# Performance work log

Hardware: AMD Instinct MI355X
Metric: run time of the kernel (lower is better)

## Reference

```python
import jax, jax.numpy as jnp
import numpy as np

D = 100  # embedding_dim (hard-coded in the original module)


def _prelu(x, a):
    return jnp.where(x >= 0, x, a * x)


def setup_inputs() -> dict:
    key = jax.random.key(0)
    ks = jax.random.split(key, 12)
    B, S, L, R, V = 32, 50, 20, 16, 50000
    T = L * R  # tokens per sentence = len_max_sentence * n_routes
    return {
        "stories": jax.random.randint(ks[0], (B, S, T), 0, V),
        "queries": jax.random.randint(ks[1], (B, L), 0, V),
        "emb": 0.1 * jax.random.normal(ks[2], (V, D), dtype=jnp.float32),
        "in_mult": jnp.ones((T, D), dtype=jnp.float32),
        "q_mult": jnp.ones((L, D), dtype=jnp.float32),
        "keys": 0.1 * jax.random.normal(ks[3], (R, D), dtype=jnp.float32),
        "init_state": 0.1 * jax.random.normal(ks[4], (D,), dtype=jnp.float32),
        "U": 0.1 * jax.random.normal(ks[5], (R * D, D), dtype=jnp.float32),
        "Vw": 0.1 * jax.random.normal(ks[6], (R * D, R * D), dtype=jnp.float32),
        "Ww": 0.1 * jax.random.normal(ks[7], (R * D, R * D), dtype=jnp.float32),
        "Hw": 0.1 * jax.random.normal(ks[8], (D, D), dtype=jnp.float32),
        "Rw": 0.1 * jax.random.normal(ks[9], (V, D), dtype=jnp.float32),
        "alpha_in": jnp.ones((1,), dtype=jnp.float32),  # PReLU(init=1)
        "alpha_q": jnp.ones((1,), dtype=jnp.float32),
    }


def reference(stories, queries, emb, in_mult, q_mult, keys, init_state,
              U, Vw, Ww, Hw, Rw, alpha_in, alpha_q):
    B, S, T = stories.shape
    R = keys.shape[0]
    emb0 = emb.at[0].set(0.0)  # padding_idx=0 row is zero
    # stories -> [B,S,T,D] -> route-sum -> [B,S,R,D]
    x = emb0[stories] * in_mult
    x = x.reshape(B, S, R, T // R, D).sum(axis=3)
    # V(keys.flatten()) is constant across timesteps
    v_keys = (keys.reshape(-1) @ Vw.T).reshape(R, D)
    state0 = jnp.tile(init_state[None, None, :], (B, 1, 1))  # [B,1,D]

    def step(state, sent):  # state [B,1,D], sent [B,R,D]
        gate = jax.nn.sigmoid(sent * state + sent * keys)
        u = (state.reshape(B, D) @ U.T).reshape(B, R, D)
        w = (sent.reshape(B, R * D) @ Ww.T).reshape(B, R, D)
        cand = _prelu(u + v_keys + w, alpha_in)
        # null-sentence mask: zero out positions where gate == sigmoid(0) = 0.5
        mask = jax.lax.stop_gradient(jnp.where(gate == 0.5, 0.0, 1.0))
        state = state + (cand * gate * mask).sum(axis=1, keepdims=True)
        # torch.norm over singleton dim=1 (= elementwise abs), kept faithful
        state = state / jnp.sqrt(jnp.sum(state * state, axis=1, keepdims=True))
        return state, None

    state, _ = jax.lax.scan(step, state0, jnp.swapaxes(x, 0, 1))

    q = (emb0[queries] * q_mult).sum(axis=1, keepdims=True)  # [B,1,D]
    h = _prelu(q + (state.reshape(B, D) @ Hw.T).reshape(B, 1, D), alpha_q)
    return h.reshape(B, D) @ Rw.T  # [B, vocab]
```

## Files before the change

### kernel.cpp

```cpp
#include <hip/hip_runtime.h>
#include <cstddef>
#include <cstdint>

#define B_  32
#define S_  50
#define L_  20
#define R_  16
#define D_  100
#define V_  50000
#define T_  320
#define RD_ 1600
#define BS_ 1600
#define NG_ 25
#define NP_ 16

typedef float v4f __attribute__((ext_vector_type(4)));
typedef unsigned short u16;
#define NTL(p)  __builtin_nontemporal_load((const v4f*)(p))

__device__ __forceinline__ float uf(unsigned u) { return __uint_as_float(u); }

__device__ __forceinline__ void bsplit(float a, unsigned& h, unsigned& l) {
  const unsigned bits = __float_as_uint(a);
  const unsigned hb = bits & 0xffff0000u;
  h = hb >> 16;
  l = __float_as_uint(a - __uint_as_float(hb)) >> 16;
}

__device__ __forceinline__ void bsplit4(float4 a, uint2& h, uint2& l) {
  unsigned h0,h1,h2,h3,l0,l1,l2,l3;
  bsplit(a.x, h0, l0); bsplit(a.y, h1, l1);
  bsplit(a.z, h2, l2); bsplit(a.w, h3, l3);
  h.x = h0 | (h1 << 16); h.y = h2 | (h3 << 16);
  l.x = l0 | (l1 << 16); l.y = l2 | (l3 << 16);
}

__global__ __launch_bounds__(512) void setup_kernel(
    const int* __restrict__ stories, const float* __restrict__ emb,
    const float* __restrict__ in_mult, const float* __restrict__ U,
    const float* __restrict__ Vw, const float* __restrict__ keys,
    const float* __restrict__ init_state, const float* __restrict__ Ww,
    float* __restrict__ x,
    u16* __restrict__ wh, u16* __restrict__ wl,
    float* __restrict__ table, float* __restrict__ vk, float* __restrict__ u0)
{
  const int blk = blockIdx.x, tid = threadIdx.x;
  if (blk < 1600) {
    __shared__ int toks[T_];
    const int* st = stories + (size_t)blk * T_;
    if (tid < T_) toks[tid] = st[tid];
    __syncthreads();
    if (tid < 400) {
      const int j4 = tid * 4;
      const int r  = j4 / D_;
      const int d4 = j4 - r * D_;
      float4 acc = make_float4(0.f, 0.f, 0.f, 0.f);
      #pragma unroll
      for (int l = 0; l < 20; ++l) {
        const int t = r * 20 + l;
        const int tok = toks[t];
        if (tok != 0) {
          float4 e = *(const float4*)&emb[(size_t)tok * D_ + d4];
          float4 m = *(const float4*)&in_mult[(size_t)t * D_ + d4];
          acc.x += e.x * m.x; acc.y += e.y * m.y;
          acc.z += e.z * m.z; acc.w += e.w * m.w;
        }
      }
      *(float4*)&x[(size_t)blk * RD_ + j4] = acc;
    }
  } else if (blk < 2000) {
    const int q = blk - 1600;
    const int g = q >> 4, p = q & 15;
    const float s0 = (p & 1) ? -1.f : 1.f;
    const float s1 = (p & 2) ? -1.f : 1.f;
    const float s2 = (p & 4) ? -1.f : 1.f;
    const float s3 = (p & 8) ? -1.f : 1.f;
    if (tid < 400) {
      const int j4 = tid * 4;
      float t[4];
      #pragma unroll
      for (int jj = 0; jj < 4; ++jj) {
        const float* ur = &U[(size_t)(j4 + jj) * D_ + 4 * g];
        t[jj] = s0*ur[0] + s1*ur[1] + s2*ur[2] + s3*ur[3];
      }
      *(float4*)&table[((size_t)(g * NP_ + p)) * RD_ + j4] =
          make_float4(t[0], t[1], t[2], t[3]);
    }
  } else if (blk < 2200) {
    const int wave = tid >> 6, lane = tid & 63;
    const int j = (blk - 2000) * 8 + wave;
    float acc = 0.f;
    for (int k = lane; k < RD_; k += 64)
      acc += keys[k] * Vw[(size_t)j * RD_ + k];
    #pragma unroll
    for (int off = 32; off > 0; off >>= 1) acc += __shfl_down(acc, off);
    if (lane == 0) vk[j] = acc;
  } else if (blk < 2400) {
    const int wave = tid >> 6, lane = tid & 63;
    const int j = (blk - 2200) * 8 + wave;
    const float* Ur = U + (size_t)j * D_;
    float acc = Ur[lane] * init_state[lane];
    if (lane < 36) acc += Ur[64 + lane] * init_state[64 + lane];
    #pragma unroll
    for (int off = 32; off > 0; off >>= 1) acc += __shfl_down(acc, off);
    if (lane == 0) u0[j] = acc;
  } else {
    const int e = ((blk - 2400) * 512 + tid) * 8;
    float4 a0 = *(const float4*)&Ww[e];
    float4 a1 = *(const float4*)&Ww[e + 4];
    uint2 h0, l0, h1, l1;
    bsplit4(a0, h0, l0);
    bsplit4(a1, h1, l1);
    uint4 hv = make_uint4(h0.x, h0.y, h1.x, h1.y);
    uint4 lv = make_uint4(l0.x, l0.y, l1.x, l1.y);
    *(uint4*)&wh[e] = hv;
    *(uint4*)&wl[e] = lv;
  }
}

typedef const __attribute__((address_space(1))) unsigned GAu;
typedef __attribute__((address_space(3))) unsigned LDSu;
#define GLL(SRC, DST) __builtin_amdgcn_global_load_lds((GAu*)(SRC), (LDSu*)(DST), 16, 0, 0)

__device__ __forceinline__ void mfma16(v4f& d, v4f a, v4f b) {
  asm("v_mfma_f32_16x16x32_bf16 %0, %1, %2, %0" : "+v"(d) : "v"(a), "v"(b));
}

__global__ __launch_bounds__(256) void gemm_mfma_kernel(
    const float* __restrict__ A,
    const u16* __restrict__ wh, const u16* __restrict__ wl,
    float* __restrict__ C)
{
  __shared__ __align__(16) char smem[2][4][8192];
  const int tid = threadIdx.x;
  const int lane = tid & 63, wid = tid >> 6;
  const int bm = blockIdx.y * 128, bn = blockIdx.x * 128;

  int ldsoff[2], srcB[2];
  #pragma unroll
  for (int i = 0; i < 2; ++i) {
    const int chunk = wid * 2 + i;
    const int row = chunk * 16 + (lane >> 2);
    const int kb = (lane & 3) * 16;
    int rb = bn + row; if (rb > 1599) rb = 1599;
    srcB[i] = rb * 3200 + kb;
    ldsoff[i] = chunk * 1024;
  }
  const char* gwh = (const char*)wh;
  const char* gwl = (const char*)wl;

  int arow[4], awofs[4];
  const int akseg = tid & 7;
  #pragma unroll
  for (int i = 0; i < 4; ++i) {
    const int r = i * 32 + (tid >> 3);
    int ra = bm + r; if (ra > 1599) ra = 1599;
    arow[i] = ra;
    awofs[i] = r * 64 + akseg * 8;
  }

  const int wm = wid >> 1, wn = wid & 1;
  const int r15 = lane & 15, q = lane >> 4;
  const int aoff = (wm * 64 + r15) * 64 + q * 16;
  const int boff = (wn * 64 + r15) * 64 + q * 16;

  v4f acc[4][4];
  #pragma unroll
  for (int i = 0; i < 4; ++i)
    #pragma unroll
    for (int j = 0; j < 4; ++j) acc[i][j] = (v4f)(0.f);

  auto stageB = [&](int buf, int kt) {
    const int kb = kt * 64;
    #pragma unroll
    for (int i = 0; i < 2; ++i) {
      GLL(gwh + srcB[i] + kb, &smem[buf][2][ldsoff[i]]);
      GLL(gwl + srcB[i] + kb, &smem[buf][3][ldsoff[i]]);
    }
  };

  float4 a4[4];

  #pragma unroll
  for (int i = 0; i < 4; ++i)
    a4[i] = *(const float4*)&A[(size_t)arow[i] * RD_ + akseg * 4];
  stageB(0, 0);
  #pragma unroll
  for (int i = 0; i < 4; ++i) {
    uint2 h, l; bsplit4(a4[i], h, l);
    *(uint2*)&smem[0][0][awofs[i]] = h;
    *(uint2*)&smem[0][1][awofs[i]] = l;
  }
  __syncthreads();

  for (int kt = 0; kt < 50; ++kt) {
    const int cur = kt & 1;
    if (kt < 49) {
      stageB(cur ^ 1, kt + 1);
      #pragma unroll
      for (int i = 0; i < 4; ++i)
        a4[i] = *(const float4*)&A[(size_t)arow[i] * RD_ + (kt + 1) * 32 + akseg * 4];
    }
    const char* s0 = &smem[cur][0][0];
    v4f ah[4], al[4], bh[4], bl[4];
    #pragma unroll
    for (int t = 0; t < 4; ++t) {
      ah[t] = *(const v4f*)(s0 +         aoff + t * 1024);
      al[t] = *(const v4f*)(s0 +  8192 + aoff + t * 1024);
      bh[t] = *(const v4f*)(s0 + 16384 + boff + t * 1024);
      bl[t] = *(const v4f*)(s0 + 24576 + boff + t * 1024);
    }
    #pragma unroll
    for (int im = 0; im < 4; ++im)
      #pragma unroll
      for (int in = 0; in < 4; ++in) {
        mfma16(acc[im][in], ah[im], bh[in]);
        mfma16(acc[im][in], ah[im], bl[in]);
        mfma16(acc[im][in], al[im], bh[in]);
      }
    if (kt < 49) {
      const int nxt = cur ^ 1;
      #pragma unroll
      for (int i = 0; i < 4; ++i) {
        uint2 h, l; bsplit4(a4[i], h, l);
        *(uint2*)&smem[nxt][0][awofs[i]] = h;
        *(uint2*)&smem[nxt][1][awofs[i]] = l;
      }
    }
    __syncthreads();
  }

  const int mb  = bm + wm * 64 + q * 4;
  const int nbq = bn + wn * 64 + r15;
  #pragma unroll
  for (int im = 0; im < 4; ++im) {
    #pragma unroll
    for (int in = 0; in < 4; ++in) {
      const int n = nbq + in * 16;
      const int m0 = mb + im * 16;
      if (n < 1600) {
        #pragma unroll
        for (int r = 0; r < 4; ++r)
          if (m0 + r < 1600)
            C[(size_t)(m0 + r) * RD_ + n] = acc[im][in][r];
      }
    }
  }
}

__global__ __launch_bounds__(512, 2) void scan_kernel(
    const float* __restrict__ x,
    const float* __restrict__ Wall,
    const float* __restrict__ table,
    const float* __restrict__ u0,
    const float* __restrict__ vkeys,
    const float* __restrict__ keys,
    const float* __restrict__ init_state,
    const float* __restrict__ alpha_in_p,
    const int*   __restrict__ queries,
    const float* __restrict__ emb,
    const float* __restrict__ q_mult,
    const float* __restrict__ Hw,
    const float* __restrict__ alpha_q_p,
    float* __restrict__ h_g)
{
  const int b = blockIdx.x, tid = threadIdx.x;
  __shared__ __align__(16) float s_state[D_];
  __shared__ __align__(16) float s_c[RD_];
  __shared__ float s_hw[D_ * 101];
  __shared__ unsigned long long s_mask[2];
  const float alpha = alpha_in_p[0];
  const bool active = (tid < 400);
  const int j4 = tid * 4;
  const int d4 = (j4 % D_);
  float4 kk = make_float4(0.f,0.f,0.f,0.f), vv = kk;
  const float* xb = x    + (size_t)b * S_ * RD_;
  const float* wb = Wall + (size_t)b * S_ * RD_;
  v4f bx[5], bw[5];
  #pragma unroll
  for (int i = 0; i < 5; ++i) { bx[i] = (v4f)(0.f); bw[i] = (v4f)(0.f); }
  if (active) {
    kk = *(const float4*)&keys[j4];
    vv = *(const float4*)&vkeys[j4];
    #pragma unroll
    for (int i = 0; i < 5; ++i) {
      bx[i] = NTL(&xb[(size_t)i * RD_ + j4]);
      bw[i] = NTL(&wb[(size_t)i * RD_ + j4]);
    }
  }
  if (tid < D_) s_state[tid] = init_state[tid];
  __syncthreads();

  for (int sg = 0; sg < S_; sg += 5) {
    #pragma unroll
    for (int i = 0; i < 5; ++i) {
      const int s = sg + i;
      if (active) {
        const v4f sent = bx[i], w = bw[i];
        if (s + 5 < S_) {
          bx[i] = NTL(&xb[(size_t)(s + 5) * RD_ + j4]);
          bw[i] = NTL(&wb[(size_t)(s + 5) * RD_ + j4]);
        }
        v4f u;
        if (s == 0) {
          float4 t0 = *(const float4*)&u0[j4];
          u.x = t0.x; u.y = t0.y; u.z = t0.z; u.w = t0.w;
        } else {
          u = (v4f)(0.f);
          const unsigned long long m0 = s_mask[0];
          const unsigned long long m1 = s_mask[1];
          #pragma unroll
          for (int g = 0; g < NG_; ++g) {
            const unsigned idx = (g < 16)
                ? (unsigned)((m0 >> (4 * g)) & 15ull)
                : (unsigned)((m1 >> (4 * g - 64)) & 15ull);
            float4 tv = *(const float4*)&table[((size_t)(g * NP_) + idx) * RD_ + j4];
            u.x += tv.x; u.y += tv.y; u.z += tv.z; u.w += tv.w;
          }
        }
        float4 sd = *(const float4*)&s_state[d4];
        float zx = sent.x * sd.x + sent.x * kk.x;
        float zy = sent.y * sd.y + sent.y * kk.y;
        float zz = sent.z * sd.z + sent.z * kk.z;
        float zw = sent.w * sd.w + sent.w * kk.w;
        float gx = 1.0f / (1.0f + expf(-zx));
        float gy = 1.0f / (1.0f + expf(-zy));
        float gz = 1.0f / (1.0f + expf(-zz));
        float gw = 1.0f / (1.0f + expf(-zw));
        float cx = u.x + vv.x + w.x; cx = cx >= 0.f ? cx : alpha * cx;
        float cy = u.y + vv.y + w.y; cy = cy >= 0.f ? cy : alpha * cy;
        float cz = u.z + vv.z + w.z; cz = cz >= 0.f ? cz : alpha * cz;
        float cw = u.w + vv.w + w.w; cw = cw >= 0.f ? cw : alpha * cw;
        v4f cc;
        cc.x = (gx == 0.5f) ? 0.f : cx * gx;
        cc.y = (gy == 0.5f) ? 0.f : cy * gy;
        cc.z = (gz == 0.5f) ? 0.f : cz * gz;
        cc.w = (gw == 0.5f) ? 0.f : cw * gw;
        *(v4f*)&s_c[j4] = cc;
      }
      __syncthreads();
      if (tid < D_) {
        float csum = 0.f;
        #pragma unroll
        for (int r = 0; r < R_; ++r) csum += s_c[r * D_ + tid];
        float v = s_state[tid] + csum;
        v = v / sqrtf(v * v);
        s_state[tid] = v;
        unsigned long long mask = __ballot(v < 0.f);
        if ((tid & 63) == 0) s_mask[tid >> 6] = mask;
      }
      __syncthreads();
    }
  }

  for (int f = tid; f < D_ * D_; f += 512) {
    const int row = f / D_, col = f - row * D_;
    s_hw[row * 101 + col] = Hw[f];
  }
  __syncthreads();
  if (tid < D_) {
    float q = 0.f;
    #pragma unroll
    for (int l = 0; l < L_; ++l) {
      const int tok = queries[b * L_ + l];
      if (tok != 0) q += emb[(size_t)tok * D_ + tid] * q_mult[l * D_ + tid];
    }
    float a = 0.f;
    #pragma unroll 4
    for (int k = 0; k < D_; ++k) a += s_state[k] * s_hw[tid * 101 + k];
    float h = q + a;
    const float aq = alpha_q_p[0];
    h = h >= 0.f ? h : aq * h;
    h_g[(size_t)b * D_ + tid] = h;
  }
}

__global__ __launch_bounds__(256) void out_kernel(
    const float* __restrict__ h_g, const float* __restrict__ Rw, float* __restrict__ out)
{
  __shared__ __align__(16) float sh[B_ * D_];
  __shared__ __align__(16) float sr[32 * D_];
  int tid = threadIdx.x;
  int v0 = blockIdx.x * 32;
  for (int i = tid; i < B_ * D_; i += 256) sh[i] = h_g[i];
  int nrows = V_ - v0; if (nrows > 32) nrows = 32;
  for (int i = tid; i < nrows * D_; i += 256) sr[i] = Rw[(size_t)v0 * D_ + i];
  __syncthreads();
  const float4* sh4 = (const float4*)sh;
  const float4* sr4 = (const float4*)sr;
  int tv = (tid & 15) * 2;
  int tb = (tid >> 4) * 2;
  float a00 = 0.f, a01 = 0.f, a10 = 0.f, a11 = 0.f;
  #pragma unroll
  for (int kc = 0; kc < 25; ++kc) {
    float4 h0 = sh4[tb * 25 + kc];
    float4 h1 = sh4[(tb + 1) * 25 + kc];
    float4 r0 = sr4[tv * 25 + kc];
    float4 r1 = sr4[(tv + 1) * 25 + kc];
    a00 += h0.x*r0.x + h0.y*r0.y + h0.z*r0.z + h0.w*r0.w;
    a01 += h0.x*r1.x + h0.y*r1.y + h0.z*r1.z + h0.w*r1.w;
    a10 += h1.x*r0.x + h1.y*r0.y + h1.z*r0.z + h1.w*r0.w;
    a11 += h1.x*r1.x + h1.y*r1.y + h1.z*r1.z + h1.w*r1.w;
  }
  if (tv < nrows) {
    out[(size_t)tb * V_ + v0 + tv] = a00;
    out[(size_t)(tb + 1) * V_ + v0 + tv] = a10;
  }
  if (tv + 1 < nrows) {
    out[(size_t)tb * V_ + v0 + tv + 1] = a01;
    out[(size_t)(tb + 1) * V_ + v0 + tv + 1] = a11;
  }
}

extern "C" void kernel_launch(void* const* d_in, const int* in_sizes, int n_in,
                              void* d_out, int out_size, void* d_ws, size_t ws_size,
                              hipStream_t stream) {
  const int*   stories    = (const int*)  d_in[0];
  const int*   queries    = (const int*)  d_in[1];
  const float* emb        = (const float*)d_in[2];
  const float* in_mult    = (const float*)d_in[3];
  const float* q_mult     = (const float*)d_in[4];
  const float* keys       = (const float*)d_in[5];
  const float* init_state = (const float*)d_in[6];
  const float* U          = (const float*)d_in[7];
  const float* Vw         = (const float*)d_in[8];
  const float* Ww         = (const float*)d_in[9];
  const float* Hw         = (const float*)d_in[10];
  const float* Rw         = (const float*)d_in[11];
  const float* alpha_in   = (const float*)d_in[12];
  const float* alpha_q    = (const float*)d_in[13];
  float* out = (float*)d_out;

  char* ws = (char*)d_ws;
  float* x     = (float*)(ws);
  float* Wall  = (float*)(ws + 10240000);
  float* table = (float*)(ws + 20480000);
  u16*   wwh   = (u16*)  (ws + 23040000);
  u16*   wwl   = (u16*)  (ws + 28160000);
  float* vk    = (float*)(ws + 33280000);
  float* u0    = (float*)(ws + 33286400);
  float* hbuf  = (float*)(ws + 33292800);

  setup_kernel<<<3025, 512, 0, stream>>>(stories, emb, in_mult, U, Vw, keys,
                                         init_state, Ww, x, wwh, wwl,
                                         table, vk, u0);
  gemm_mfma_kernel<<<dim3(13, 13), 256, 0, stream>>>(x, wwh, wwl, Wall);
  scan_kernel<<<B_, 512, 0, stream>>>(x, Wall, table, u0, vk, keys, init_state,
                                      alpha_in, queries, emb, q_mult, Hw, alpha_q,
                                      hbuf);
  out_kernel<<<(V_ + 31) / 32, 256, 0, stream>>>(hbuf, Rw, out);
}
```

Baseline: 386.3 us.

## Use 8 waves per GEMM block and reorder prefetch loads in scan

The bf16-split MFMA GEMM now runs 512 threads per 128x128 tile, arranged as 2x4 waves that each own a 64x32 sub-tile. This halves per-thread accumulators and staging work and doubles the waves available to hide latency across the 169 blocks. The scan kernel drops the nontemporal loads and moves the next-sentence prefetch after the gate computation, behind a sched_barrier, so it does not delay the current step's critical path. The larger blocks may lower the blocks resident per CU and add LDS read traffic for A.

Result: faster. 370.9 us (-4.0%).

```diff
diff --git a/kernel.cpp b/kernel.cpp
--- a/kernel.cpp
+++ b/kernel.cpp
@@ -16,7 +16,6 @@
 
 typedef float v4f __attribute__((ext_vector_type(4)));
 typedef unsigned short u16;
-#define NTL(p)  __builtin_nontemporal_load((const v4f*)(p))
 
 __device__ __forceinline__ float uf(unsigned u) { return __uint_as_float(u); }
 
@@ -126,7 +125,7 @@
   asm("v_mfma_f32_16x16x32_bf16 %0, %1, %2, %0" : "+v"(d) : "v"(a), "v"(b));
 }
 
-__global__ __launch_bounds__(256) void gemm_mfma_kernel(
+__global__ __launch_bounds__(512) void gemm_mfma_kernel(
     const float* __restrict__ A,
     const u16* __restrict__ wh, const u16* __restrict__ wl,
     float* __restrict__ C)
@@ -136,57 +135,49 @@
   const int lane = tid & 63, wid = tid >> 6;
   const int bm = blockIdx.y * 128, bn = blockIdx.x * 128;
 
-  int ldsoff[2], srcB[2];
-  #pragma unroll
-  for (int i = 0; i < 2; ++i) {
-    const int chunk = wid * 2 + i;
-    const int row = chunk * 16 + (lane >> 2);
-    const int kb = (lane & 3) * 16;
-    int rb = bn + row; if (rb > 1599) rb = 1599;
-    srcB[i] = rb * 3200 + kb;
-    ldsoff[i] = chunk * 1024;
-  }
+  const int brow = wid * 16 + (lane >> 2);
+  const int bkb  = (lane & 3) * 16;
+  int rb = bn + brow; if (rb > 1599) rb = 1599;
+  const int srcB = rb * 3200 + bkb;
+  const int ldsB = wid * 1024;
   const char* gwh = (const char*)wh;
   const char* gwl = (const char*)wl;
 
-  int arow[4], awofs[4];
+  int arow[2], awofs[2];
   const int akseg = tid & 7;
   #pragma unroll
-  for (int i = 0; i < 4; ++i) {
-    const int r = i * 32 + (tid >> 3);
+  for (int i = 0; i < 2; ++i) {
+    const int r = i * 64 + (tid >> 3);
     int ra = bm + r; if (ra > 1599) ra = 1599;
     arow[i] = ra;
     awofs[i] = r * 64 + akseg * 8;
   }
 
-  const int wm = wid >> 1, wn = wid & 1;
+  const int wm = wid >> 2, wn = wid & 3;
   const int r15 = lane & 15, q = lane >> 4;
   const int aoff = (wm * 64 + r15) * 64 + q * 16;
-  const int boff = (wn * 64 + r15) * 64 + q * 16;
-
-  v4f acc[4][4];
+  const int boff = (wn * 32 + r15) * 64 + q * 16;
+
+  v4f acc[4][2];
   #pragma unroll
   for (int i = 0; i < 4; ++i)
     #pragma unroll
-    for (int j = 0; j < 4; ++j) acc[i][j] = (v4f)(0.f);
+    for (int j = 0; j < 2; ++j) acc[i][j] = (v4f)(0.f);
 
   auto stageB = [&](int buf, int kt) {
     const int kb = kt * 64;
-    #pragma unroll
-    for (int i = 0; i < 2; ++i) {
-      GLL(gwh + srcB[i] + kb, &smem[buf][2][ldsoff[i]]);
-      GLL(gwl + srcB[i] + kb, &smem[buf][3][ldsoff[i]]);
-    }
+    GLL(gwh + srcB + kb, &smem[buf][2][ldsB]);
+    GLL(gwl + srcB + kb, &smem[buf][3][ldsB]);
   };
 
-  float4 a4[4];
-
-  #pragma unroll
-  for (int i = 0; i < 4; ++i)
+  float4 a4[2];
+
+  #pragma unroll
+  for (int i = 0; i < 2; ++i)
     a4[i] = *(const float4*)&A[(size_t)arow[i] * RD_ + akseg * 4];
   stageB(0, 0);
   #pragma unroll
-  for (int i = 0; i < 4; ++i) {
+  for (int i = 0; i < 2; ++i) {
     uint2 h, l; bsplit4(a4[i], h, l);
     *(uint2*)&smem[0][0][awofs[i]] = h;
     *(uint2*)&smem[0][1][awofs[i]] = l;
@@ -198,22 +189,25 @@
     if (kt < 49) {
       stageB(cur ^ 1, kt + 1);
       #pragma unroll
-      for (int i = 0; i < 4; ++i)
+      for (int i = 0; i < 2; ++i)
         a4[i] = *(const float4*)&A[(size_t)arow[i] * RD_ + (kt + 1) * 32 + akseg * 4];
     }
     const char* s0 = &smem[cur][0][0];
-    v4f ah[4], al[4], bh[4], bl[4];
+    v4f ah[4], al[4], bh[2], bl[2];
     #pragma unroll
     for (int t = 0; t < 4; ++t) {
       ah[t] = *(const v4f*)(s0 +         aoff + t * 1024);
       al[t] = *(const v4f*)(s0 +  8192 + aoff + t * 1024);
+    }
+    #pragma unroll
+    for (int t = 0; t < 2; ++t) {
       bh[t] = *(const v4f*)(s0 + 16384 + boff + t * 1024);
       bl[t] = *(const v4f*)(s0 + 24576 + boff + t * 1024);
     }
     #pragma unroll
     for (int im = 0; im < 4; ++im)
       #pragma unroll
-      for (int in = 0; in < 4; ++in) {
+      for (int in = 0; in < 2; ++in) {
         mfma16(acc[im][in], ah[im], bh[in]);
         mfma16(acc[im][in], ah[im], bl[in]);
         mfma16(acc[im][in], al[im], bh[in]);
@@ -221,7 +215,7 @@
     if (kt < 49) {
       const int nxt = cur ^ 1;
       #pragma unroll
-      for (int i = 0; i < 4; ++i) {
+      for (int i = 0; i < 2; ++i) {
         uint2 h, l; bsplit4(a4[i], h, l);
         *(uint2*)&smem[nxt][0][awofs[i]] = h;
         *(uint2*)&smem[nxt][1][awofs[i]] = l;
@@ -231,11 +225,11 @@
   }
 
   const int mb  = bm + wm * 64 + q * 4;
-  const int nbq = bn + wn * 64 + r15;
+  const int nbq = bn + wn * 32 + r15;
   #pragma unroll
   for (int im = 0; im < 4; ++im) {
     #pragma unroll
-    for (int in = 0; in < 4; ++in) {
+    for (int in = 0; in < 2; ++in) {
       const int n = nbq + in * 16;
       const int m0 = mb + im * 16;
       if (n < 1600) {
@@ -284,8 +278,8 @@
     vv = *(const float4*)&vkeys[j4];
     #pragma unroll
     for (int i = 0; i < 5; ++i) {
-      bx[i] = NTL(&xb[(size_t)i * RD_ + j4]);
-      bw[i] = NTL(&wb[(size_t)i * RD_ + j4]);
+      bx[i] = *(const v4f*)&xb[(size_t)i * RD_ + j4];
+      bw[i] = *(const v4f*)&wb[(size_t)i * RD_ + j4];
     }
   }
   if (tid < D_) s_state[tid] = init_state[tid];
@@ -297,10 +291,6 @@
       const int s = sg + i;
       if (active) {
         const v4f sent = bx[i], w = bw[i];
-        if (s + 5 < S_) {
-          bx[i] = NTL(&xb[(size_t)(s + 5) * RD_ + j4]);
-          bw[i] = NTL(&wb[(size_t)(s + 5) * RD_ + j4]);
-        }
         v4f u;
         if (s == 0) {
           float4 t0 = *(const float4*)&u0[j4];
@@ -336,6 +326,11 @@
         cc.y = (gy == 0.5f) ? 0.f : cy * gy;
         cc.z = (gz == 0.5f) ? 0.f : cz * gz;
         cc.w = (gw == 0.5f) ? 0.f : cw * gw;
+        __builtin_amdgcn_sched_barrier(0);
+        if (s + 5 < S_) {
+          bx[i] = *(const v4f*)&xb[(size_t)(s + 5) * RD_ + j4];
+          bw[i] = *(const v4f*)&wb[(size_t)(s + 5) * RD_ + j4];
+        }
         *(v4f*)&s_c[j4] = cc;
       }
       __syncthreads();
@@ -444,7 +439,7 @@
   setup_kernel<<<3025, 512, 0, stream>>>(stories, emb, in_mult, U, Vw, keys,
                                          init_state, Ww, x, wwh, wwl,
                                          table, vk, u0);
-  gemm_mfma_kernel<<<dim3(13, 13), 256, 0, stream>>>(x, wwh, wwl, Wall);
+  gemm_mfma_kernel<<<dim3(13, 13), 512, 0, stream>>>(x, wwh, wwl, Wall);
   scan_kernel<<<B_, 512, 0, stream>>>(x, Wall, table, u0, vk, keys, init_state,
                                       alpha_in, queries, emb, q_mult, Hw, alpha_q,
                                       hbuf);
```
